# Kernel optimization log

Measured on AMD Instinct MI355X. Metric: run time of the kernel, lower is better.

Reference implementation:

```python
import jax, jax.numpy as jnp
import numpy as np

N_NODES = 50000
D_IN = 128
D_OUT = 128
N_EDGES = 800000


def setup_inputs() -> dict:
    key = jax.random.key(0)
    k1, k2, k3, k4 = jax.random.split(key, 4)
    x = jax.random.normal(k1, (N_NODES, D_IN), dtype=jnp.float32)
    # nn.Linear(input_size, output_size, bias=False): weight is [out, in], y = x @ W.T.
    # We store W1 as [in, out] so y = x @ W1 (same math, transposed storage).
    W1 = jax.random.normal(k2, (D_IN, D_OUT), dtype=jnp.float32) * (1.0 / np.sqrt(D_IN))
    row = jax.random.randint(k3, (N_EDGES,), 0, N_NODES, dtype=jnp.int64)
    col = jax.random.randint(k4, (N_EDGES,), 0, N_NODES, dtype=jnp.int64)
    edge_index = jnp.stack([row, col], axis=0)  # [2, E]
    return {"x": x, "W1": W1, "edge_index": edge_index}


def reference(x, W1, edge_index):
    # Linear transform: [N, D_in] @ [D_in, D_out] -> [N, D_out]
    norm_m = x @ W1
    adj_row = edge_index[0]  # source nodes (gather)
    adj_col = edge_index[1]  # destination nodes (scatter)
    gathered = norm_m[adj_row]  # [E, D_out]
    pooled = jax.ops.segment_max(gathered, adj_col, num_segments=x.shape[0])
    # torch_scatter fills segments with no incoming edges with 0 (not -inf)
    deg = jax.ops.segment_sum(jnp.ones_like(adj_col, dtype=jnp.int32), adj_col,
                              num_segments=x.shape[0])
    pooled = jnp.where((deg > 0)[:, None], pooled, jnp.zeros_like(pooled))
    return jnp.concatenate((x, pooled), axis=1)  # [N, D_in + D_out]
```

## Files before the change

kernel.cpp:

```cpp
#include <hip/hip_runtime.h>


#define N_DIN 128
#define CAP 64

typedef __attribute__((ext_vector_type(8))) short bf16x8;
typedef __attribute__((ext_vector_type(4))) float f32x4;

__device__ __forceinline__ short f32_bf16(float f) {
    unsigned u = __float_as_uint(f);
    return (short)((u + 0x7fffu + ((u >> 16) & 1u)) >> 16);
}

__global__ __launch_bounds__(256) void wconv(const float* __restrict__ W,
                                             short* __restrict__ Wt) {
    int i = blockIdx.x * 256 + threadIdx.x;
    int k = i >> 5, n0 = (i & 31) * 4;
    float4 v = *(const float4*)(W + k * 128 + n0);
    Wt[(n0 + 0) * 128 + k] = f32_bf16(v.x);
    Wt[(n0 + 1) * 128 + k] = f32_bf16(v.y);
    Wt[(n0 + 2) * 128 + k] = f32_bf16(v.z);
    Wt[(n0 + 3) * 128 + k] = f32_bf16(v.w);
}

__global__ __launch_bounds__(256) void fused_gemm_scatter(
        const float* __restrict__ X, const short* __restrict__ Wt,
        short* __restrict__ Yb, float* __restrict__ out, int N, int gblocks,
        const int* __restrict__ row, const int* __restrict__ col,
        int* __restrict__ cur, unsigned short* __restrict__ csrc, int E) {
    if ((int)blockIdx.x >= gblocks) {
        int e = ((int)blockIdx.x - gblocks) * 256 + (int)threadIdx.x;
        if (e < E) {
            int dst = col[e];
            int pos = atomicAdd(&cur[dst], 1);
            if (pos < CAP)
                csrc[dst * CAP + pos] = (unsigned short)row[e];
        }
        return;
    }
    __shared__ short c_lds[4][32][128];
    const int tid = threadIdx.x;
    const int w = tid >> 6, l = tid & 63;
    const int lr = l & 15, lg = l >> 4;
    const int R0 = (int)blockIdx.x * 128 + w * 32;

    bf16x8 af[2][4];
#pragma unroll
    for (int rt = 0; rt < 2; ++rt) {
        int gr = R0 + rt * 16 + lr;
        int grc = gr < N ? gr : N - 1;
#pragma unroll
        for (int t = 0; t < 4; ++t) {
            int kc = t * 32 + lg * 8;
            float4 v0 = *(const float4*)(X + (size_t)grc * 128 + kc);
            float4 v1 = *(const float4*)(X + (size_t)grc * 128 + kc + 4);
            if (gr < N) {
                *(float4*)(out + (size_t)gr * 256 + kc)     = v0;
                *(float4*)(out + (size_t)gr * 256 + kc + 4) = v1;
            }
            bf16x8 a;
            a[0] = f32_bf16(v0.x); a[1] = f32_bf16(v0.y);
            a[2] = f32_bf16(v0.z); a[3] = f32_bf16(v0.w);
            a[4] = f32_bf16(v1.x); a[5] = f32_bf16(v1.y);
            a[6] = f32_bf16(v1.z); a[7] = f32_bf16(v1.w);
            af[rt][t] = a;
        }
    }
#pragma unroll
    for (int ct = 0; ct < 8; ++ct) {
        f32x4 c0 = {0.f, 0.f, 0.f, 0.f}, c1 = {0.f, 0.f, 0.f, 0.f};
        const short* bp = Wt + (ct * 16 + lr) * 128;
#pragma unroll
        for (int t = 0; t < 4; ++t) {
            bf16x8 b = *(const bf16x8*)(bp + t * 32 + lg * 8);
            c0 = __builtin_amdgcn_mfma_f32_16x16x32_bf16(af[0][t], b, c0, 0, 0, 0);
            c1 = __builtin_amdgcn_mfma_f32_16x16x32_bf16(af[1][t], b, c1, 0, 0, 0);
        }
#pragma unroll
        for (int i = 0; i < 4; ++i) {
            c_lds[w][lg * 4 + i][ct * 16 + lr]      = f32_bf16(c0[i]);
            c_lds[w][16 + lg * 4 + i][ct * 16 + lr] = f32_bf16(c1[i]);
        }
    }
#pragma unroll
    for (int it = 0; it < 8; ++it) {
        int cid = it * 64 + l;
        int r2 = cid >> 4, c2 = cid & 15;
        int gr = R0 + r2;
        if (gr < N) {
            bf16x8 vv = *(const bf16x8*)(&c_lds[w][r2][c2 * 8]);
            *(bf16x8*)(Yb + (size_t)gr * 128 + c2 * 8) = vv;
        }
    }
}

__global__ __launch_bounds__(256) void pool_bf16(const unsigned* __restrict__ nmb,
                                                 const int* __restrict__ cur,
                                                 const unsigned short* __restrict__ csrc,
                                                 float* __restrict__ out, int N) {
    int node = blockIdx.x * 4 + (threadIdx.x >> 6);
    if (node >= N) return;
    int lane = threadIdx.x & 63;
    int deg = cur[node];
    if (deg > CAP) deg = CAP;
    const unsigned short* lst = csrc + node * CAP;
    float2 acc = make_float2(-INFINITY, -INFINITY);
    int j = 0;
    for (; j + 4 <= deg; j += 4) {
        int s0 = lst[j], s1 = lst[j + 1], s2 = lst[j + 2], s3 = lst[j + 3];
        unsigned v0 = nmb[s0 * 64 + lane];
        unsigned v1 = nmb[s1 * 64 + lane];
        unsigned v2 = nmb[s2 * 64 + lane];
        unsigned v3 = nmb[s3 * 64 + lane];
        acc.x = fmaxf(acc.x, fmaxf(fmaxf(__uint_as_float(v0 << 16), __uint_as_float(v1 << 16)),
                                   fmaxf(__uint_as_float(v2 << 16), __uint_as_float(v3 << 16))));
        acc.y = fmaxf(acc.y, fmaxf(fmaxf(__uint_as_float(v0 & 0xffff0000u), __uint_as_float(v1 & 0xffff0000u)),
                                   fmaxf(__uint_as_float(v2 & 0xffff0000u), __uint_as_float(v3 & 0xffff0000u))));
    }
    for (; j < deg; ++j) {
        unsigned v0 = nmb[lst[j] * 64 + lane];
        acc.x = fmaxf(acc.x, __uint_as_float(v0 << 16));
        acc.y = fmaxf(acc.y, __uint_as_float(v0 & 0xffff0000u));
    }
    if (deg == 0) acc = make_float2(0.f, 0.f);
    *(float2*)(out + (size_t)node * 256 + N_DIN + lane * 2) = acc;
}

extern "C" void kernel_launch(void* const* d_in, const int* in_sizes, int n_in,
                              void* d_out, int out_size, void* d_ws, size_t ws_size,
                              hipStream_t stream) {
    const float* x  = (const float*)d_in[0];
    const float* W1 = (const float*)d_in[1];
    const int* ei   = (const int*)d_in[2];
    const int N = in_sizes[0] / N_DIN;
    const int E = in_sizes[2] / 2;
    const int* row = ei;
    const int* col = ei + E;
    float* out = (float*)d_out;

    short* norm_mb = (short*)d_ws;
    short* Wt = norm_mb + (size_t)N * N_DIN;
    int* cur  = (int*)(Wt + 128 * 128);
    unsigned short* csrc = (unsigned short*)(cur + N);

    const int gblocks = (N + 127) / 128;
    const int sblocks = (E + 255) / 256;

    hipMemsetAsync(cur, 0, (size_t)N * sizeof(int), stream);
    wconv<<<16, 256, 0, stream>>>(W1, Wt);
    fused_gemm_scatter<<<gblocks + sblocks, 256, 0, stream>>>(
        x, Wt, norm_mb, out, N, gblocks, row, col, cur, csrc, E);
    pool_bf16<<<(N + 3) / 4, 256, 0, stream>>>((const unsigned*)norm_mb, cur, csrc, out, N);
}
```

Baseline: 168.6 us.

## Fold memset into weight prep, batch scatter atomics, shuffle-broadcast neighbor lists

Replaces the separate hipMemsetAsync with zeroing of the degree counters inside the weight-conversion kernel, which removes one launch. The scatter blocks now handle four edges per thread and issue their atomics back to back, so more atomic traffic is in flight per thread. The pool kernel loads each node's 64-entry neighbor list with one coalesced read per wave and hands indices to lanes with __shfl, instead of each lane reading every list entry. The prep grid grows to cover N threads, and the scatter uses fewer, larger blocks.

```diff
diff --git a/kernel.cpp b/kernel.cpp
--- a/kernel.cpp
+++ b/kernel.cpp
@@ -12,29 +12,45 @@
     return (short)((u + 0x7fffu + ((u >> 16) & 1u)) >> 16);
 }
 
-__global__ __launch_bounds__(256) void wconv(const float* __restrict__ W,
-                                             short* __restrict__ Wt) {
+__global__ __launch_bounds__(256) void prep_k(const float* __restrict__ W,
+                                              short* __restrict__ Wt,
+                                              int* __restrict__ cur, int N) {
     int i = blockIdx.x * 256 + threadIdx.x;
-    int k = i >> 5, n0 = (i & 31) * 4;
-    float4 v = *(const float4*)(W + k * 128 + n0);
-    Wt[(n0 + 0) * 128 + k] = f32_bf16(v.x);
-    Wt[(n0 + 1) * 128 + k] = f32_bf16(v.y);
-    Wt[(n0 + 2) * 128 + k] = f32_bf16(v.z);
-    Wt[(n0 + 3) * 128 + k] = f32_bf16(v.w);
+    if (i < 4096) {
+        int k = i >> 5, n0 = (i & 31) * 4;
+        float4 v = *(const float4*)(W + k * 128 + n0);
+        Wt[(n0 + 0) * 128 + k] = f32_bf16(v.x);
+        Wt[(n0 + 1) * 128 + k] = f32_bf16(v.y);
+        Wt[(n0 + 2) * 128 + k] = f32_bf16(v.z);
+        Wt[(n0 + 3) * 128 + k] = f32_bf16(v.w);
+    }
+    if (i < N) cur[i] = 0;
 }
 
-__global__ __launch_bounds__(256) void fused_gemm_scatter(
-        const float* __restrict__ X, const short* __restrict__ Wt,
-        short* __restrict__ Yb, float* __restrict__ out, int N, int gblocks,
-        const int* __restrict__ row, const int* __restrict__ col,
-        int* __restrict__ cur, unsigned short* __restrict__ csrc, int E) {
+__global__ __launch_bounds__(256) void fused_k(const float* __restrict__ X,
+                                               const short* __restrict__ Wt,
+                                               short* __restrict__ Yb,
+                                               float* __restrict__ out, int N, int gblocks,
+                                               const int* __restrict__ row,
+                                               const int* __restrict__ col,
+                                               int* __restrict__ cur,
+                                               unsigned short* __restrict__ csrc, int E) {
     if ((int)blockIdx.x >= gblocks) {
-        int e = ((int)blockIdx.x - gblocks) * 256 + (int)threadIdx.x;
-        if (e < E) {
-            int dst = col[e];
-            int pos = atomicAdd(&cur[dst], 1);
-            if (pos < CAP)
-                csrc[dst * CAP + pos] = (unsigned short)row[e];
+        int base = ((int)blockIdx.x - gblocks) * 1024 + (int)threadIdx.x;
+        int d[4], p[4];
+#pragma unroll
+        for (int i = 0; i < 4; ++i) {
+            int e = base + i * 256;
+            d[i] = (e < E) ? col[e] : -1;
+        }
+#pragma unroll
+        for (int i = 0; i < 4; ++i)
+            p[i] = (d[i] >= 0) ? atomicAdd(&cur[d[i]], 1) : CAP;
+#pragma unroll
+        for (int i = 0; i < 4; ++i) {
+            int e = base + i * 256;
+            if (d[i] >= 0 && p[i] < CAP)
+                csrc[d[i] * CAP + p[i]] = (unsigned short)row[e];
         }
         return;
     }
@@ -94,20 +110,23 @@
     }
 }
 
-__global__ __launch_bounds__(256) void pool_bf16(const unsigned* __restrict__ nmb,
-                                                 const int* __restrict__ cur,
-                                                 const unsigned short* __restrict__ csrc,
-                                                 float* __restrict__ out, int N) {
+__global__ __launch_bounds__(256) void pool_k(const unsigned* __restrict__ nmb,
+                                              const int* __restrict__ cur,
+                                              const unsigned short* __restrict__ csrc,
+                                              float* __restrict__ out, int N) {
     int node = blockIdx.x * 4 + (threadIdx.x >> 6);
     if (node >= N) return;
     int lane = threadIdx.x & 63;
     int deg = cur[node];
     if (deg > CAP) deg = CAP;
-    const unsigned short* lst = csrc + node * CAP;
+    int mysrc = csrc[node * CAP + lane];
     float2 acc = make_float2(-INFINITY, -INFINITY);
     int j = 0;
     for (; j + 4 <= deg; j += 4) {
-        int s0 = lst[j], s1 = lst[j + 1], s2 = lst[j + 2], s3 = lst[j + 3];
+        int s0 = __shfl(mysrc, j,     64);
+        int s1 = __shfl(mysrc, j + 1, 64);
+        int s2 = __shfl(mysrc, j + 2, 64);
+        int s3 = __shfl(mysrc, j + 3, 64);
         unsigned v0 = nmb[s0 * 64 + lane];
         unsigned v1 = nmb[s1 * 64 + lane];
         unsigned v2 = nmb[s2 * 64 + lane];
@@ -118,7 +137,8 @@
                                    fmaxf(__uint_as_float(v2 & 0xffff0000u), __uint_as_float(v3 & 0xffff0000u))));
     }
     for (; j < deg; ++j) {
-        unsigned v0 = nmb[lst[j] * 64 + lane];
+        int s0 = __shfl(mysrc, j, 64);
+        unsigned v0 = nmb[s0 * 64 + lane];
         acc.x = fmaxf(acc.x, __uint_as_float(v0 << 16));
         acc.y = fmaxf(acc.y, __uint_as_float(v0 & 0xffff0000u));
     }
@@ -144,11 +164,10 @@
     unsigned short* csrc = (unsigned short*)(cur + N);
 
     const int gblocks = (N + 127) / 128;
-    const int sblocks = (E + 255) / 256;
+    const int sblocks = (E + 1023) / 1024;
 
-    hipMemsetAsync(cur, 0, (size_t)N * sizeof(int), stream);
-    wconv<<<16, 256, 0, stream>>>(W1, Wt);
-    fused_gemm_scatter<<<gblocks + sblocks, 256, 0, stream>>>(
-        x, Wt, norm_mb, out, N, gblocks, row, col, cur, csrc, E);
-    pool_bf16<<<(N + 3) / 4, 256, 0, stream>>>((const unsigned*)norm_mb, cur, csrc, out, N);
+    prep_k<<<(N + 255) / 256, 256, 0, stream>>>(W1, Wt, cur, N);
+    fused_k<<<gblocks + sblocks, 256, 0, stream>>>(x, Wt, norm_mb, out, N, gblocks,
+                                                   row, col, cur, csrc, E);
+    pool_k<<<(N + 3) / 4, 256, 0, stream>>>((const unsigned*)norm_mb, cur, csrc, out, N);
 }
```

New measurement: 169.7 us. Within noise of the previous version (+0.7%).
